# Optimization experiments

Hardware: AMD Instinct MI355X
Metric: run time of the kernel (lower is better)

Reference implementation:

```python
import jax, jax.numpy as jnp
import numpy as np

L = 10   # lattice side (hardcoded self.length)
K = 3    # kernel_size -> half_k = 1 wrap padding
FN = 4   # filter_num
B = 262144


def setup_inputs() -> dict:
    key = jax.random.key(0)
    k1, k2, k3, k4, k5 = jax.random.split(key, 5)
    v = jax.random.normal(k1, (B, L * L), dtype=jnp.float32)
    # torch default init scale ~ 1/sqrt(fan_in)
    conv_w = jax.random.normal(k2, (FN, 1, K, K), dtype=jnp.float32) / 3.0
    conv_b = jax.random.normal(k3, (FN,), dtype=jnp.float32) * 0.1
    deconv_w = jax.random.normal(k4, (FN, 1, 2, 2), dtype=jnp.float32) / 4.0
    deconv_b = jax.random.normal(k5, (1,), dtype=jnp.float32) * 0.1
    data = jnp.zeros((1,), dtype=jnp.int32)  # unused positional arg of log_psi
    return {"v": v, "conv_w": conv_w, "conv_b": conv_b,
            "deconv_w": deconv_w, "deconv_b": deconv_b, "data": data}


def _log_psi(v, conv_w, conv_b, deconv_w, deconv_b):
    b = v.shape[0]
    x = v.reshape(b, 1, L, L)
    # handmade_padding == periodic (wrap) pad of width half_k=1 on both spatial axes
    x = jnp.pad(x, ((0, 0), (0, 0), (1, 1), (1, 1)), mode="wrap")  # [B,1,12,12]
    # Conv2d(1, FN, 3), VALID -> [B,FN,10,10]
    y = jax.lax.conv_general_dilated(
        x, conv_w, window_strides=(1, 1), padding="VALID",
        dimension_numbers=("NCHW", "OIHW", "NCHW"))
    y = y + conv_b[None, :, None, None]
    # MaxPool2d(2,2): non-overlapping 2x2 -> [B,FN,5,5]
    y = y.reshape(b, FN, L // 2, 2, L // 2, 2).max(axis=(3, 5))
    # ConvTranspose2d(FN,1,kernel=2,stride=2): each input pixel -> disjoint 2x2 block
    # torch weight layout [in=FN, out=1, 2, 2]
    z = jnp.einsum("bcij,cokl->boikjl", y, deconv_w).reshape(b, 1, L, L)
    z = z + deconv_b[None, :, None, None]
    sign_z = jnp.sign(z)
    abs_z = z * sign_z
    sign_prod = sign_z.reshape(b, -1).prod(axis=1)        # scalar per sample
    log_sum = jnp.log(abs_z).reshape(b, -1).sum(axis=1)   # scalar per sample
    return sign_prod, log_sum


def reference(v, conv_w, conv_b, deconv_w, deconv_b, data):
    return _log_psi(v, conv_w, conv_b, deconv_w, deconv_b)
```

## Files before the change

kernel.cpp:

```cpp
#include <hip/hip_runtime.h>
#include <math.h>


typedef float v2f __attribute__((ext_vector_type(2)));

#define SREAD(x) __int_as_float(__builtin_amdgcn_readfirstlane(__float_as_int(x)))

__device__ __forceinline__ float dpp_swap1_f(float x) {
    return __int_as_float(__builtin_amdgcn_mov_dpp(__float_as_int(x), 0xB1, 0xF, 0xF, true));
}
__device__ __forceinline__ unsigned dpp_swap1_u(unsigned x) {
    return (unsigned)__builtin_amdgcn_mov_dpp((int)x, 0xB1, 0xF, 0xF, true);
}

__device__ __forceinline__ void gload16(const float* g, float* l) {
    __builtin_amdgcn_global_load_lds(
        (const __attribute__((address_space(1))) void*)g,
        (__attribute__((address_space(3))) void*)l, 16, 0, 0);
}
__device__ __forceinline__ void gload4(const float* g, float* l) {
    __builtin_amdgcn_global_load_lds(
        (const __attribute__((address_space(1))) void*)g,
        (__attribute__((address_space(3))) void*)l, 4, 0, 0);
}

__global__ __launch_bounds__(256) void CNN2D_37495064494620_kernel(
    const float* __restrict__ v,
    const float* __restrict__ cw,
    const float* __restrict__ cb,
    const float* __restrict__ dw,
    const float* __restrict__ db,
    float* __restrict__ out,
    int B)
{
    const int tid = threadIdx.x;
    const int q   = tid & 1;
    const int sl  = tid >> 1;

    __shared__ __align__(16) float sm[12800];

    const float* gbase = v + (size_t)blockIdx.x * 12800;
    const int widx = tid >> 6;
    #pragma unroll
    for (int k = 0; k < 12; ++k)
        gload16(gbase + k * 1024 + tid * 4, &sm[k * 1024 + widx * 256]);
    #pragma unroll
    for (int k = 0; k < 2; ++k)
        gload4(gbase + 12288 + k * 256 + tid, &sm[12288 + k * 256 + widx * 64]);

    float Wf[4][9];
    #pragma unroll
    for (int f = 0; f < 4; ++f)
        #pragma unroll
        for (int t = 0; t < 9; ++t)
            Wf[f][t] = SREAD(cw[f * 9 + t]);
    v2f W2[9][2];
    #pragma unroll
    for (int t = 0; t < 9; ++t) {
        W2[t][0] = (v2f){Wf[0][t], Wf[1][t]};
        W2[t][1] = (v2f){Wf[2][t], Wf[3][t]};
    }
    const v2f Cb2[2] = { (v2f){SREAD(cb[0]), SREAD(cb[1])},
                         (v2f){SREAD(cb[2]), SREAD(cb[3])} };
    float Dw[4][4];
    #pragma unroll
    for (int f = 0; f < 4; ++f)
        #pragma unroll
        for (int t = 0; t < 4; ++t)
            Dw[f][t] = SREAD(dw[f * 4 + t]);
    const float Db = SREAD(db[0]);

    v2f Dq[4];
    #pragma unroll
    for (int f = 0; f < 4; ++f)
        Dq[f] = (v2f){ q ? Dw[f][2] : Dw[f][0], q ? Dw[f][3] : Dw[f][1] };

    __syncthreads();

    const float* my = sm + sl * 100;

    unsigned sbits = 0u;
    float l2 = 0.0f;

    #pragma unroll
    for (int i = 0; i < 5; ++i) {
        const int r1 = 2 * i + q;
        const int r0 = (i == 0) ? (q ? 0 : 9) : (2 * i - 1 + q);
        const int r2 = (i == 4) ? (q ? 0 : 9) : (2 * i + 1 + q);

        float R[3][10];
        #pragma unroll
        for (int t = 0; t < 5; ++t) {
            float2 x0 = *(const float2*)(my + r0 * 10 + 2 * t);
            float2 x1 = *(const float2*)(my + r1 * 10 + 2 * t);
            float2 x2 = *(const float2*)(my + r2 * 10 + 2 * t);
            R[0][2 * t] = x0.x; R[0][2 * t + 1] = x0.y;
            R[1][2 * t] = x1.x; R[1][2 * t + 1] = x1.y;
            R[2][2 * t] = x2.x; R[2][2 * t + 1] = x2.y;
        }

        #pragma unroll
        for (int j = 0; j < 5; ++j) {
            v2f a0[2] = {Cb2[0], Cb2[1]};
            v2f a1[2] = {Cb2[0], Cb2[1]};
            #pragma unroll
            for (int kr = 0; kr < 3; ++kr) {
                #pragma unroll
                for (int kc = 0; kc < 3; ++kc) {
                    const int cc0 = (2 * j + kc + 9) % 10;
                    const int cc1 = (2 * j + 1 + kc + 9) % 10;
                    const int t = kr * 3 + kc;
                    const v2f x0 = (v2f){R[kr][cc0], R[kr][cc0]};
                    const v2f x1 = (v2f){R[kr][cc1], R[kr][cc1]};
                    a0[0] = __builtin_elementwise_fma(x0, W2[t][0], a0[0]);
                    a0[1] = __builtin_elementwise_fma(x0, W2[t][1], a0[1]);
                    a1[0] = __builtin_elementwise_fma(x1, W2[t][0], a1[0]);
                    a1[1] = __builtin_elementwise_fma(x1, W2[t][1], a1[1]);
                }
            }
            const v2f m0 = __builtin_elementwise_max(a0[0], a1[0]);
            const v2f m1 = __builtin_elementwise_max(a0[1], a1[1]);
            float P[4];
            P[0] = fmaxf(m0.x, dpp_swap1_f(m0.x));
            P[1] = fmaxf(m0.y, dpp_swap1_f(m0.y));
            P[2] = fmaxf(m1.x, dpp_swap1_f(m1.x));
            P[3] = fmaxf(m1.y, dpp_swap1_f(m1.y));

            v2f z2 = (v2f){Db, Db};
            #pragma unroll
            for (int f = 0; f < 4; ++f) {
                const v2f pf = (v2f){P[f], P[f]};
                z2 = __builtin_elementwise_fma(pf, Dq[f], z2);
            }
            sbits ^= __float_as_uint(z2.x) ^ __float_as_uint(z2.y);
            l2 += __log2f(fabsf(z2.x * z2.y));
        }
    }

    l2 = l2 + dpp_swap1_f(l2);
    sbits = sbits ^ dpp_swap1_u(sbits);

    const int s = blockIdx.x * 128 + sl;
    const float val = q ? (l2 * 0.69314718055994531f)
                        : ((sbits & 0x80000000u) ? -1.0f : 1.0f);
    out[q * B + s] = val;
}

extern "C" void kernel_launch(void* const* d_in, const int* in_sizes, int n_in,
                              void* d_out, int out_size, void* d_ws, size_t ws_size,
                              hipStream_t stream) {
    const float* v  = (const float*)d_in[0];
    const float* cw = (const float*)d_in[1];
    const float* cb = (const float*)d_in[2];
    const float* dw = (const float*)d_in[3];
    const float* db = (const float*)d_in[4];
    float* out = (float*)d_out;

    const int B = in_sizes[0] / 100;
    const int grid = B / 128;
    CNN2D_37495064494620_kernel<<<grid, 256, 0, stream>>>(v, cw, cb, dw, db, out, B);
}
```

Baseline: 169.3 us.

## Split samples across four lanes and double-buffer per-wave LDS staging

Each sample is now handled by four lanes instead of two, with each lane computing two of the four filters, and a second DPP swap combines the pooled values across lane pairs. Each 64-lane wave owns a private two-slot LDS buffer and streams its 64 samples in four chunks of 16. It waits on vmcnt so the global-to-LDS load of the next chunk overlaps compute on the current one, with no block barrier. Blocks shrink to 128 threads, and per-lane FMA work is halved at the cost of more lanes per sample and extra cross-lane shuffles. The hand-placed waitcnt asm and the LDS slot reuse after lgkmcnt are fragile if the compiler reorders memory operations.

```diff
diff --git a/kernel.cpp b/kernel.cpp
--- a/kernel.cpp
+++ b/kernel.cpp
@@ -5,12 +5,21 @@
 typedef float v2f __attribute__((ext_vector_type(2)));
 
 #define SREAD(x) __int_as_float(__builtin_amdgcn_readfirstlane(__float_as_int(x)))
+#define WAITVM(N) asm volatile("s_waitcnt vmcnt(" #N ")" ::: "memory")
+#define WAITLGKM0() asm volatile("s_waitcnt lgkmcnt(0)" ::: "memory")
+#define MEMFENCE() asm volatile("" ::: "memory")
 
 __device__ __forceinline__ float dpp_swap1_f(float x) {
     return __int_as_float(__builtin_amdgcn_mov_dpp(__float_as_int(x), 0xB1, 0xF, 0xF, true));
 }
+__device__ __forceinline__ float dpp_swap2_f(float x) {
+    return __int_as_float(__builtin_amdgcn_mov_dpp(__float_as_int(x), 0x4E, 0xF, 0xF, true));
+}
 __device__ __forceinline__ unsigned dpp_swap1_u(unsigned x) {
     return (unsigned)__builtin_amdgcn_mov_dpp((int)x, 0xB1, 0xF, 0xF, true);
+}
+__device__ __forceinline__ unsigned dpp_swap2_u(unsigned x) {
+    return (unsigned)__builtin_amdgcn_mov_dpp((int)x, 0x4E, 0xF, 0xF, true);
 }
 
 __device__ __forceinline__ void gload16(const float* g, float* l) {
@@ -24,7 +33,7 @@
         (__attribute__((address_space(3))) void*)l, 4, 0, 0);
 }
 
-__global__ __launch_bounds__(256) void CNN2D_37495064494620_kernel(
+__global__ __launch_bounds__(128, 3) void CNN2D_37495064494620_kernel(
     const float* __restrict__ v,
     const float* __restrict__ cw,
     const float* __restrict__ cb,
@@ -33,20 +42,14 @@
     float* __restrict__ out,
     int B)
 {
-    const int tid = threadIdx.x;
-    const int q   = tid & 1;
-    const int sl  = tid >> 1;
+    const int lane = threadIdx.x & 63;
+    const int w    = threadIdx.x >> 6;
+    const int q    = lane & 1;
+    const int h    = (lane >> 1) & 1;
+    const int g    = lane >> 2;
 
-    __shared__ __align__(16) float sm[12800];
-
-    const float* gbase = v + (size_t)blockIdx.x * 12800;
-    const int widx = tid >> 6;
-    #pragma unroll
-    for (int k = 0; k < 12; ++k)
-        gload16(gbase + k * 1024 + tid * 4, &sm[k * 1024 + widx * 256]);
-    #pragma unroll
-    for (int k = 0; k < 2; ++k)
-        gload4(gbase + 12288 + k * 256 + tid, &sm[12288 + k * 256 + widx * 64]);
+    __shared__ __align__(16) float smraw[6400];
+    float* sm = smraw + w * 3200;
 
     float Wf[4][9];
     #pragma unroll
@@ -54,96 +57,118 @@
         #pragma unroll
         for (int t = 0; t < 9; ++t)
             Wf[f][t] = SREAD(cw[f * 9 + t]);
-    v2f W2[9][2];
+    v2f Wsel[9];
     #pragma unroll
-    for (int t = 0; t < 9; ++t) {
-        W2[t][0] = (v2f){Wf[0][t], Wf[1][t]};
-        W2[t][1] = (v2f){Wf[2][t], Wf[3][t]};
-    }
-    const v2f Cb2[2] = { (v2f){SREAD(cb[0]), SREAD(cb[1])},
-                         (v2f){SREAD(cb[2]), SREAD(cb[3])} };
-    float Dw[4][4];
+    for (int t = 0; t < 9; ++t)
+        Wsel[t] = (v2f){ h ? Wf[2][t] : Wf[0][t], h ? Wf[3][t] : Wf[1][t] };
+    const float cb0 = SREAD(cb[0]), cb1 = SREAD(cb[1]);
+    const float cb2 = SREAD(cb[2]), cb3 = SREAD(cb[3]);
+    const v2f Cbsel = (v2f){ h ? cb2 : cb0, h ? cb3 : cb1 };
+
+    float Dw4[4][4];
     #pragma unroll
     for (int f = 0; f < 4; ++f)
         #pragma unroll
         for (int t = 0; t < 4; ++t)
-            Dw[f][t] = SREAD(dw[f * 4 + t]);
+            Dw4[f][t] = SREAD(dw[f * 4 + t]);
     const float Db = SREAD(db[0]);
+    float Dkl[4];
+    #pragma unroll
+    for (int f = 0; f < 4; ++f) {
+        const float e01 = h ? Dw4[f][1] : Dw4[f][0];
+        const float e23 = h ? Dw4[f][3] : Dw4[f][2];
+        Dkl[f] = q ? e23 : e01;
+    }
+    const float Ds0 = h ? Dkl[2] : Dkl[0];
+    const float Ds1 = h ? Dkl[3] : Dkl[1];
+    const float Ds2 = h ? Dkl[0] : Dkl[2];
+    const float Ds3 = h ? Dkl[1] : Dkl[3];
 
-    v2f Dq[4];
-    #pragma unroll
-    for (int f = 0; f < 4; ++f)
-        Dq[f] = (v2f){ q ? Dw[f][2] : Dw[f][0], q ? Dw[f][3] : Dw[f][1] };
+    WAITVM(0);
 
-    __syncthreads();
+    const float* gbase = v + (size_t)blockIdx.x * 12800 + w * 6400;
 
-    const float* my = sm + sl * 100;
+    auto STAGE = [&](int b) {
+        const float* gb = gbase + b * 1600;
+        float* lb = sm + (b & 1) * 1600;
+        #pragma unroll
+        for (int k = 0; k < 6; ++k)
+            gload16(gb + k * 256 + lane * 4, lb + k * 256);
+        gload4(gb + 1536 + lane, lb + 1536);
+    };
 
-    unsigned sbits = 0u;
-    float l2 = 0.0f;
+    STAGE(0);
+    MEMFENCE();
+    STAGE(1);
 
-    #pragma unroll
-    for (int i = 0; i < 5; ++i) {
-        const int r1 = 2 * i + q;
-        const int r0 = (i == 0) ? (q ? 0 : 9) : (2 * i - 1 + q);
-        const int r2 = (i == 4) ? (q ? 0 : 9) : (2 * i + 1 + q);
+    #pragma unroll 1
+    for (int b = 0; b < 4; ++b) {
+        if (b < 3) WAITVM(7); else WAITVM(0);
 
-        float R[3][10];
+        const float* my = sm + (b & 1) * 1600 + g * 100;
+        unsigned sb = 0u;
+        float l2 = 0.0f;
+
         #pragma unroll
-        for (int t = 0; t < 5; ++t) {
-            float2 x0 = *(const float2*)(my + r0 * 10 + 2 * t);
-            float2 x1 = *(const float2*)(my + r1 * 10 + 2 * t);
-            float2 x2 = *(const float2*)(my + r2 * 10 + 2 * t);
-            R[0][2 * t] = x0.x; R[0][2 * t + 1] = x0.y;
-            R[1][2 * t] = x1.x; R[1][2 * t + 1] = x1.y;
-            R[2][2 * t] = x2.x; R[2][2 * t + 1] = x2.y;
+        for (int i = 0; i < 5; ++i) {
+            const int r1 = 2 * i + q;
+            const int r0 = (i == 0) ? (q ? 0 : 9) : (2 * i - 1 + q);
+            const int r2 = (i == 4) ? (q ? 0 : 9) : (2 * i + 1 + q);
+
+            float R[3][10];
+            #pragma unroll
+            for (int t = 0; t < 5; ++t) {
+                float2 x0 = *(const float2*)(my + r0 * 10 + 2 * t);
+                float2 x1 = *(const float2*)(my + r1 * 10 + 2 * t);
+                float2 x2 = *(const float2*)(my + r2 * 10 + 2 * t);
+                R[0][2 * t] = x0.x; R[0][2 * t + 1] = x0.y;
+                R[1][2 * t] = x1.x; R[1][2 * t + 1] = x1.y;
+                R[2][2 * t] = x2.x; R[2][2 * t + 1] = x2.y;
+            }
+
+            #pragma unroll
+            for (int j = 0; j < 5; ++j) {
+                v2f a0 = Cbsel, a1 = Cbsel;
+                #pragma unroll
+                for (int kr = 0; kr < 3; ++kr) {
+                    #pragma unroll
+                    for (int kc = 0; kc < 3; ++kc) {
+                        const int cc0 = (2 * j + kc + 9) % 10;
+                        const int cc1 = (2 * j + 1 + kc + 9) % 10;
+                        const int t = kr * 3 + kc;
+                        const v2f x0 = (v2f){R[kr][cc0], R[kr][cc0]};
+                        const v2f x1 = (v2f){R[kr][cc1], R[kr][cc1]};
+                        a0 = __builtin_elementwise_fma(x0, Wsel[t], a0);
+                        a1 = __builtin_elementwise_fma(x1, Wsel[t], a1);
+                    }
+                }
+                const v2f m = __builtin_elementwise_max(a0, a1);
+                const float Px = fmaxf(m.x, dpp_swap1_f(m.x));
+                const float Py = fmaxf(m.y, dpp_swap1_f(m.y));
+                const float Qx = dpp_swap2_f(Px);
+                const float Qy = dpp_swap2_f(Py);
+                float z = Db;
+                z = fmaf(Px, Ds0, z);
+                z = fmaf(Py, Ds1, z);
+                z = fmaf(Qx, Ds2, z);
+                z = fmaf(Qy, Ds3, z);
+                sb ^= __float_as_uint(z);
+                l2 += __log2f(fabsf(z));
+            }
         }
 
-        #pragma unroll
-        for (int j = 0; j < 5; ++j) {
-            v2f a0[2] = {Cb2[0], Cb2[1]};
-            v2f a1[2] = {Cb2[0], Cb2[1]};
-            #pragma unroll
-            for (int kr = 0; kr < 3; ++kr) {
-                #pragma unroll
-                for (int kc = 0; kc < 3; ++kc) {
-                    const int cc0 = (2 * j + kc + 9) % 10;
-                    const int cc1 = (2 * j + 1 + kc + 9) % 10;
-                    const int t = kr * 3 + kc;
-                    const v2f x0 = (v2f){R[kr][cc0], R[kr][cc0]};
-                    const v2f x1 = (v2f){R[kr][cc1], R[kr][cc1]};
-                    a0[0] = __builtin_elementwise_fma(x0, W2[t][0], a0[0]);
-                    a0[1] = __builtin_elementwise_fma(x0, W2[t][1], a0[1]);
-                    a1[0] = __builtin_elementwise_fma(x1, W2[t][0], a1[0]);
-                    a1[1] = __builtin_elementwise_fma(x1, W2[t][1], a1[1]);
-                }
-            }
-            const v2f m0 = __builtin_elementwise_max(a0[0], a1[0]);
-            const v2f m1 = __builtin_elementwise_max(a0[1], a1[1]);
-            float P[4];
-            P[0] = fmaxf(m0.x, dpp_swap1_f(m0.x));
-            P[1] = fmaxf(m0.y, dpp_swap1_f(m0.y));
-            P[2] = fmaxf(m1.x, dpp_swap1_f(m1.x));
-            P[3] = fmaxf(m1.y, dpp_swap1_f(m1.y));
+        l2 += dpp_swap1_f(l2);
+        l2 += dpp_swap2_f(l2);
+        sb ^= dpp_swap1_u(sb);
+        sb ^= dpp_swap2_u(sb);
 
-            v2f z2 = (v2f){Db, Db};
-            #pragma unroll
-            for (int f = 0; f < 4; ++f) {
-                const v2f pf = (v2f){P[f], P[f]};
-                z2 = __builtin_elementwise_fma(pf, Dq[f], z2);
-            }
-            sbits ^= __float_as_uint(z2.x) ^ __float_as_uint(z2.y);
-            l2 += __log2f(fabsf(z2.x * z2.y));
-        }
+        const int s = blockIdx.x * 128 + w * 64 + b * 16 + g;
+        const int r = lane & 3;
+        if (r == 0)      out[s]     = (sb & 0x80000000u) ? -1.0f : 1.0f;
+        else if (r == 1) out[B + s] = l2 * 0.69314718055994531f;
+
+        if (b < 2) { WAITLGKM0(); STAGE(b + 2); }
     }
-
-    l2 = l2 + dpp_swap1_f(l2);
-    sbits = sbits ^ dpp_swap1_u(sbits);
-
-    const int s = blockIdx.x * 128 + sl;
-    const float val = q ? (l2 * 0.69314718055994531f)
-                        : ((sbits & 0x80000000u) ? -1.0f : 1.0f);
-    out[q * B + s] = val;
 }
 
 extern "C" void kernel_launch(void* const* d_in, const int* in_sizes, int n_in,
@@ -158,5 +183,5 @@
 
     const int B = in_sizes[0] / 100;
     const int grid = B / 128;
-    CNN2D_37495064494620_kernel<<<grid, 256, 0, stream>>>(v, cw, cb, dw, db, out, B);
+    CNN2D_37495064494620_kernel<<<grid, 128, 0, stream>>>(v, cw, cb, dw, db, out, B);
 }
```

New measurement: 180.6 us. 1.07x slower.

## Load rows directly into registers and share halo rows via DPP swaps

Applied to the files above, without the earlier changes.

Removes the LDS staging buffer and the block barrier. Each lane now loads its five rows (even or odd by parity) straight from global memory into registers, and the neighbouring halo rows come from the partner lane through DPP lane swaps instead of LDS reads. It also sets launch bounds to 3 blocks per CU and computes the sign from the product of the pair. The risks are higher register pressure from holding 50 floats per lane, and strided per-lane global loads that may coalesce less well than the earlier bulk global-to-LDS copies.

```diff
diff --git a/kernel.cpp b/kernel.cpp
--- a/kernel.cpp
+++ b/kernel.cpp
@@ -13,18 +13,7 @@
     return (unsigned)__builtin_amdgcn_mov_dpp((int)x, 0xB1, 0xF, 0xF, true);
 }
 
-__device__ __forceinline__ void gload16(const float* g, float* l) {
-    __builtin_amdgcn_global_load_lds(
-        (const __attribute__((address_space(1))) void*)g,
-        (__attribute__((address_space(3))) void*)l, 16, 0, 0);
-}
-__device__ __forceinline__ void gload4(const float* g, float* l) {
-    __builtin_amdgcn_global_load_lds(
-        (const __attribute__((address_space(1))) void*)g,
-        (__attribute__((address_space(3))) void*)l, 4, 0, 0);
-}
-
-__global__ __launch_bounds__(256) void CNN2D_37495064494620_kernel(
+__global__ __launch_bounds__(256, 3) void CNN2D_37495064494620_kernel(
     const float* __restrict__ v,
     const float* __restrict__ cw,
     const float* __restrict__ cb,
@@ -33,20 +22,23 @@
     float* __restrict__ out,
     int B)
 {
-    const int tid = threadIdx.x;
-    const int q   = tid & 1;
-    const int sl  = tid >> 1;
+    const int lane = threadIdx.x & 63;
+    const int wv   = threadIdx.x >> 6;
+    const int q    = lane & 1;
+    const int sl   = lane >> 1;
+    const int s    = blockIdx.x * 128 + wv * 32 + sl;
 
-    __shared__ __align__(16) float sm[12800];
-
-    const float* gbase = v + (size_t)blockIdx.x * 12800;
-    const int widx = tid >> 6;
+    const float* my = v + (size_t)s * 100;
+    float R[5][10];
     #pragma unroll
-    for (int k = 0; k < 12; ++k)
-        gload16(gbase + k * 1024 + tid * 4, &sm[k * 1024 + widx * 256]);
-    #pragma unroll
-    for (int k = 0; k < 2; ++k)
-        gload4(gbase + 12288 + k * 256 + tid, &sm[12288 + k * 256 + widx * 64]);
+    for (int k = 0; k < 5; ++k) {
+        const float* rp = my + (2 * k + q) * 10;
+        #pragma unroll
+        for (int t = 0; t < 5; ++t) {
+            const float2 x = *(const float2*)(rp + 2 * t);
+            R[k][2 * t] = x.x; R[k][2 * t + 1] = x.y;
+        }
+    }
 
     float Wf[4][9];
     #pragma unroll
@@ -62,42 +54,40 @@
     }
     const v2f Cb2[2] = { (v2f){SREAD(cb[0]), SREAD(cb[1])},
                          (v2f){SREAD(cb[2]), SREAD(cb[3])} };
-    float Dw[4][4];
+    float Dw4[4][4];
     #pragma unroll
     for (int f = 0; f < 4; ++f)
         #pragma unroll
         for (int t = 0; t < 4; ++t)
-            Dw[f][t] = SREAD(dw[f * 4 + t]);
+            Dw4[f][t] = SREAD(dw[f * 4 + t]);
     const float Db = SREAD(db[0]);
-
     v2f Dq[4];
     #pragma unroll
     for (int f = 0; f < 4; ++f)
-        Dq[f] = (v2f){ q ? Dw[f][2] : Dw[f][0], q ? Dw[f][3] : Dw[f][1] };
+        Dq[f] = (v2f){ q ? Dw4[f][2] : Dw4[f][0], q ? Dw4[f][3] : Dw4[f][1] };
 
-    __syncthreads();
-
-    const float* my = sm + sl * 100;
+    float X0[10], X1[10];
+    #pragma unroll
+    for (int e = 0; e < 10; ++e) {
+        const float t = q ? R[4][e] : R[0][e];
+        X0[e] = dpp_swap1_f(t);
+    }
 
     unsigned sbits = 0u;
     float l2 = 0.0f;
 
     #pragma unroll
     for (int i = 0; i < 5; ++i) {
-        const int r1 = 2 * i + q;
-        const int r0 = (i == 0) ? (q ? 0 : 9) : (2 * i - 1 + q);
-        const int r2 = (i == 4) ? (q ? 0 : 9) : (2 * i + 1 + q);
-
-        float R[3][10];
+        float* Xp = (i & 1) ? X1 : X0;
+        float* Xn = (i & 1) ? X0 : X1;
         #pragma unroll
-        for (int t = 0; t < 5; ++t) {
-            float2 x0 = *(const float2*)(my + r0 * 10 + 2 * t);
-            float2 x1 = *(const float2*)(my + r1 * 10 + 2 * t);
-            float2 x2 = *(const float2*)(my + r2 * 10 + 2 * t);
-            R[0][2 * t] = x0.x; R[0][2 * t + 1] = x0.y;
-            R[1][2 * t] = x1.x; R[1][2 * t + 1] = x1.y;
-            R[2][2 * t] = x2.x; R[2][2 * t + 1] = x2.y;
+        for (int e = 0; e < 10; ++e) {
+            const float t = q ? R[i][e] : R[(i + 1) % 5][e];
+            Xn[e] = dpp_swap1_f(t);
         }
+        const float* R0 = Xp;
+        const float* R1 = R[i];
+        const float* R2 = Xn;
 
         #pragma unroll
         for (int j = 0; j < 5; ++j) {
@@ -105,13 +95,14 @@
             v2f a1[2] = {Cb2[0], Cb2[1]};
             #pragma unroll
             for (int kr = 0; kr < 3; ++kr) {
+                const float* Rr = (kr == 0) ? R0 : ((kr == 1) ? R1 : R2);
                 #pragma unroll
                 for (int kc = 0; kc < 3; ++kc) {
                     const int cc0 = (2 * j + kc + 9) % 10;
                     const int cc1 = (2 * j + 1 + kc + 9) % 10;
                     const int t = kr * 3 + kc;
-                    const v2f x0 = (v2f){R[kr][cc0], R[kr][cc0]};
-                    const v2f x1 = (v2f){R[kr][cc1], R[kr][cc1]};
+                    const v2f x0 = (v2f){Rr[cc0], Rr[cc0]};
+                    const v2f x1 = (v2f){Rr[cc1], Rr[cc1]};
                     a0[0] = __builtin_elementwise_fma(x0, W2[t][0], a0[0]);
                     a0[1] = __builtin_elementwise_fma(x0, W2[t][1], a0[1]);
                     a1[0] = __builtin_elementwise_fma(x1, W2[t][0], a1[0]);
@@ -132,18 +123,17 @@
                 const v2f pf = (v2f){P[f], P[f]};
                 z2 = __builtin_elementwise_fma(pf, Dq[f], z2);
             }
-            sbits ^= __float_as_uint(z2.x) ^ __float_as_uint(z2.y);
-            l2 += __log2f(fabsf(z2.x * z2.y));
+            const float zp = z2.x * z2.y;
+            sbits ^= __float_as_uint(zp);
+            l2 += __log2f(fabsf(zp));
         }
     }
 
     l2 = l2 + dpp_swap1_f(l2);
     sbits = sbits ^ dpp_swap1_u(sbits);
 
-    const int s = blockIdx.x * 128 + sl;
-    const float val = q ? (l2 * 0.69314718055994531f)
-                        : ((sbits & 0x80000000u) ? -1.0f : 1.0f);
-    out[q * B + s] = val;
+    if (q == 0) out[s]     = (sbits & 0x80000000u) ? -1.0f : 1.0f;
+    else        out[B + s] = l2 * 0.69314718055994531f;
 }
 
 extern "C" void kernel_launch(void* const* d_in, const int* in_sizes, int n_in,
```

After: 172.2 us. Within noise of the previous version (+1.7%).
